# Performance work log

Hardware: AMD Instinct MI355X
Metric: run time of the kernel (lower is better)

The kernel has to match this reference:

```python
import jax, jax.numpy as jnp
import numpy as np

N = 100_000      # nodes
E = 1_600_000    # edges (avg degree 16)
D_IN, D_H, D_OUT = 128, 128, 64


def setup_inputs() -> dict:
    key = jax.random.key(0)
    ks = jax.random.split(key, 6)
    x = jax.random.normal(ks[0], (N, D_IN), jnp.float32)
    edge_index = jax.random.randint(ks[1], (2, E), 0, N, dtype=jnp.int32)
    W1 = jax.random.normal(ks[2], (D_IN, D_H), jnp.float32) / np.sqrt(D_IN)
    b1 = jnp.zeros((D_H,), jnp.float32)
    W2 = jax.random.normal(ks[3], (D_H, D_OUT), jnp.float32) / np.sqrt(D_H)
    b2 = jnp.zeros((D_OUT,), jnp.float32)
    return {"x": x, "edge_index": edge_index, "W1": W1, "b1": b1, "W2": W2, "b2": b2}


def _gcn_layer(x, W, b, src, dst, n_nodes):
    # PyG GCNConv: h = x @ W; symmetric norm with self-loops; scatter-add; + bias
    h = x @ W                                        # [N, D_out]
    deg = jax.ops.segment_sum(jnp.ones_like(dst, jnp.float32), dst,
                              num_segments=n_nodes)  # self-loops => deg >= 1
    dinv = jax.lax.rsqrt(deg)                        # deg^{-1/2}
    norm = dinv[src] * dinv[dst]                     # [E+N]
    msg = h[src] * norm[:, None]                     # gather + scale
    out = jax.ops.segment_sum(msg, dst, num_segments=n_nodes)  # scatter-add
    return out + b


def reference(x, edge_index, W1, b1, W2, b2):
    n = x.shape[0]
    loop = jnp.arange(n, dtype=edge_index.dtype)
    src = jnp.concatenate([edge_index[0], loop])     # add self-loops
    dst = jnp.concatenate([edge_index[1], loop])
    h = _gcn_layer(x, W1, b1, src, dst, n)
    h = jax.nn.relu(h)
    # dropout(p=0.5) is identity in eval mode
    out = _gcn_layer(h, W2, b2, src, dst, n)
    return out
```

## Files before the change

### kernel.cpp

```cpp
#include <hip/hip_runtime.h>
#include <hip/hip_bf16.h>


#define NTHREADS 256
#define BSH 9
#define NBMAX 256

typedef unsigned int uint;
typedef unsigned short ushort;
typedef __attribute__((ext_vector_type(8))) short short8;
typedef __attribute__((ext_vector_type(4))) float floatx4;

__device__ __forceinline__ uint pack_bf16(float a, float b) {
    __hip_bfloat162 h = __float22bfloat162_rn(make_float2(a, b));
    return *reinterpret_cast<uint*>(&h);
}
__device__ __forceinline__ float bf16_lo(uint q) { return __uint_as_float(q << 16); }
__device__ __forceinline__ float bf16_hi(uint q) { return __uint_as_float(q & 0xffff0000u); }

__global__ __launch_bounds__(256) void bucket_hist_kernel(
    const int* __restrict__ dst, int* __restrict__ bcnt, int e, int nb) {
    __shared__ int hist[NBMAX];
    int t = threadIdx.x;
    for (int b = t; b < nb; b += 256) hist[b] = 0;
    __syncthreads();
    int e0 = blockIdx.x * 2048;
#pragma unroll
    for (int v = 0; v < 2; v++) {
        int gi = e0 + t * 8 + v * 4;
        if (gi + 3 < e) {
            int4 d4 = *(const int4*)&dst[gi];
            atomicAdd(&hist[d4.x >> BSH], 1);
            atomicAdd(&hist[d4.y >> BSH], 1);
            atomicAdd(&hist[d4.z >> BSH], 1);
            atomicAdd(&hist[d4.w >> BSH], 1);
        } else {
            for (int j = 0; j < 4; j++)
                if (gi + j < e) atomicAdd(&hist[dst[gi + j] >> BSH], 1);
        }
    }
    __syncthreads();
    for (int b = t; b < nb; b += 256) {
        int v = hist[b];
        if (v) atomicAdd(&bcnt[b], v);
    }
}

__global__ void bucket_scan(const int* __restrict__ bcnt, int* __restrict__ bstart,
                            int* __restrict__ bcursor, int nb) {
    __shared__ int buf[NBMAX];
    int t = threadIdx.x;
    int v = (t < nb) ? bcnt[t] : 0;
    buf[t] = v;
    __syncthreads();
    int x = v;
    for (int off = 1; off < NBMAX; off <<= 1) {
        int y = (t >= off) ? buf[t - off] : 0;
        __syncthreads();
        x += y;
        buf[t] = x;
        __syncthreads();
    }
    if (t < nb) {
        bstart[t] = x - v;
        bcursor[t] = x - v;
    }
}

__global__ __launch_bounds__(256) void partition_kernel(
    const int* __restrict__ src, const int* __restrict__ dst,
    int* __restrict__ bcursor, int2* __restrict__ staged, int e, int nb) {
    __shared__ int eS[2048];
    __shared__ int eD[2048];
    __shared__ int hist[NBMAX];
    __shared__ int base[NBMAX];
    int t = threadIdx.x;
    int e0 = blockIdx.x * 2048;

    for (int b = t; b < nb; b += 256) hist[b] = 0;
    __syncthreads();
#pragma unroll
    for (int v = 0; v < 2; v++) {
        int li = t * 8 + v * 4;
        int gi = e0 + li;
        int4 s4, d4;
        if (gi + 3 < e) {
            s4 = *(const int4*)&src[gi];
            d4 = *(const int4*)&dst[gi];
        } else {
            const int* sp = &src[gi];
            const int* dp = &dst[gi];
            s4.x = (gi + 0 < e) ? sp[0] : 0;  d4.x = (gi + 0 < e) ? dp[0] : -1;
            s4.y = (gi + 1 < e) ? sp[1] : 0;  d4.y = (gi + 1 < e) ? dp[1] : -1;
            s4.z = (gi + 2 < e) ? sp[2] : 0;  d4.z = (gi + 2 < e) ? dp[2] : -1;
            s4.w = (gi + 3 < e) ? sp[3] : 0;  d4.w = (gi + 3 < e) ? dp[3] : -1;
        }
        *(int4*)&eS[li] = s4;
        *(int4*)&eD[li] = d4;
        if (d4.x >= 0) atomicAdd(&hist[d4.x >> BSH], 1);
        if (d4.y >= 0) atomicAdd(&hist[d4.y >> BSH], 1);
        if (d4.z >= 0) atomicAdd(&hist[d4.z >> BSH], 1);
        if (d4.w >= 0) atomicAdd(&hist[d4.w >> BSH], 1);
    }
    __syncthreads();
    for (int b = t; b < nb; b += 256) {
        int v = hist[b];
        base[b] = v ? atomicAdd(&bcursor[b], v) : 0;
        hist[b] = 0;
    }
    __syncthreads();
#pragma unroll
    for (int i = 0; i < 8; i++) {
        int li = t + i * 256;
        int d = eD[li];
        if (d >= 0) {
            int b = d >> BSH;
            int r = atomicAdd(&hist[b], 1);
            staged[base[b] + r] = make_int2(eS[li], d);
        }
    }
}

__global__ __launch_bounds__(256) void fine_count_kernel(
    const int2* __restrict__ staged, const int* __restrict__ bstart,
    const int* __restrict__ bcnt, int* __restrict__ cnt,
    int* __restrict__ startA, float* __restrict__ dinv, int n) {
    __shared__ int lcnt[512];
    __shared__ int tsum[256];
    int b = blockIdx.x;
    int t = threadIdx.x;
    lcnt[t] = 0;
    lcnt[t + 256] = 0;
    __syncthreads();
    int s0 = bstart[b];
    int m = bcnt[b];
    for (int i = t; i < m; i += 256)
        atomicAdd(&lcnt[staged[s0 + i].y & 511], 1);
    __syncthreads();
    int v0 = lcnt[2 * t];
    int v1 = lcnt[2 * t + 1];
    int tot = v0 + v1;
    tsum[t] = tot;
    __syncthreads();
    int x = tot;
    for (int off = 1; off < 256; off <<= 1) {
        int y = (t >= off) ? tsum[t - off] : 0;
        __syncthreads();
        x += y;
        tsum[t] = x;
        __syncthreads();
    }
    int excl = x - tot;
    int node = (b << BSH) + 2 * t;
    if (node < n) {
        cnt[node] = v0;
        startA[node] = s0 + excl;
        dinv[node] = rsqrtf((float)v0 + 1.0f);
    }
    if (node + 1 < n) {
        cnt[node + 1] = v1;
        startA[node + 1] = s0 + excl + v0;
        dinv[node + 1] = rsqrtf((float)v1 + 1.0f);
    }
}

__global__ __launch_bounds__(256) void fine_fill_kernel(
    const int2* __restrict__ staged, const int* __restrict__ bstart,
    const int* __restrict__ bcnt, const int* __restrict__ startA,
    const float* __restrict__ dinv, int2* __restrict__ rec, int n) {
    __shared__ int lcur[512];
    __shared__ float ldv[512];
    int b = blockIdx.x;
    int t = threadIdx.x;
    int nb0 = b << BSH;
    for (int i = t; i < 512; i += 256) {
        int node = nb0 + i;
        lcur[i] = (node < n) ? startA[node] : 0;
        ldv[i] = (node < n) ? dinv[node] : 0.f;
    }
    __syncthreads();
    int s0 = bstart[b];
    int m = bcnt[b];
    for (int i = t; i < m; i += 256) {
        int2 ed = staged[s0 + i];
        int li = ed.y & 511;
        int pos = atomicAdd(&lcur[li], 1);
        float nw = dinv[ed.x] * ldv[li];
        rec[pos] = make_int2(ed.x, __float_as_int(nw));
    }
}

template <int COLS, bool XF32>
__global__ __launch_bounds__(256) void gemm_mfma(const void* __restrict__ Xv,
                                                 const float* __restrict__ W,
                                                 uint* __restrict__ Cq, int n) {
    __shared__ ushort sX[64 * 128];
    __shared__ ushort sWT[COLS * 128];
    int t = threadIdx.x;
    int rbase = blockIdx.x * 64;

    if (XF32) {
        const float* X = (const float*)Xv;
#pragma unroll
        for (int i = 0; i < 8; i++) {
            int f = t + 256 * i;
            int r = f >> 5;
            int c4 = f & 31;
            float4 v = make_float4(0.f, 0.f, 0.f, 0.f);
            int gr = rbase + r;
            if (gr < n) v = *(const float4*)(X + (size_t)gr * 128 + c4 * 4);
            uint lo = pack_bf16(v.x, v.y);
            uint hi = pack_bf16(v.z, v.w);
            int chunk = c4 >> 1;
            int sub = (c4 & 1) * 4;
            int off = r * 128 + (((chunk ^ (r & 15)) << 3) + sub);
            *(uint2*)&sX[off] = make_uint2(lo, hi);
        }
    } else {
        const ushort* X = (const ushort*)Xv;
#pragma unroll
        for (int i = 0; i < 4; i++) {
            int f = t + 256 * i;
            int r = f >> 4;
            int chunk = f & 15;
            uint4 v = make_uint4(0, 0, 0, 0);
            int gr = rbase + r;
            if (gr < n) v = *(const uint4*)(X + (size_t)gr * 128 + chunk * 8);
            int off = r * 128 + ((chunk ^ (r & 15)) << 3);
            *(uint4*)&sX[off] = v;
        }
    }
    {
        constexpr int UNITS = 64 * (COLS / 4);
        constexpr int PER_T = UNITS / 256;
#pragma unroll
        for (int i = 0; i < PER_T; i++) {
            int u = t + 256 * i;
            int kp = u / (COLS / 4);
            int n4 = u % (COLS / 4);
            int k = kp * 2;
            float4 w0 = *(const float4*)(W + (size_t)k * COLS + n4 * 4);
            float4 w1 = *(const float4*)(W + (size_t)(k + 1) * COLS + n4 * 4);
            int chunk = k >> 3;
            int sub = k & 7;
            const float* a0 = (const float*)&w0;
            const float* a1 = (const float*)&w1;
#pragma unroll
            for (int j = 0; j < 4; j++) {
                int nn = n4 * 4 + j;
                uint pk = pack_bf16(a0[j], a1[j]);
                int off = nn * 128 + (((chunk ^ (nn & 15)) << 3) + sub);
                *(uint*)&sWT[off] = pk;
            }
        }
    }
    __syncthreads();

    int lane = t & 63;
    int wave = t >> 6;
    int m = lane & 15;
    int q = lane >> 4;
    int r0 = wave * 16;

    floatx4 acc[COLS / 16];
#pragma unroll
    for (int c = 0; c < COLS / 16; c++) acc[c] = (floatx4){0.f, 0.f, 0.f, 0.f};

#pragma unroll
    for (int ks = 0; ks < 4; ks++) {
        int rr = r0 + m;
        int ca = (ks * 4 + q) ^ (rr & 15);
        short8 afrag = *(const short8*)&sX[rr * 128 + (ca << 3)];
#pragma unroll
        for (int c = 0; c < COLS / 16; c++) {
            int nn = c * 16 + m;
            int cb = (ks * 4 + q) ^ (nn & 15);
            short8 bfrag = *(const short8*)&sWT[nn * 128 + (cb << 3)];
            acc[c] = __builtin_amdgcn_mfma_f32_16x16x32_bf16(bfrag, afrag, acc[c], 0, 0, 0);
        }
    }

    int gr = rbase + r0 + m;
    if (gr < n) {
#pragma unroll
        for (int c = 0; c < COLS / 16; c++) {
            uint2 pk;
            pk.x = pack_bf16(acc[c][0], acc[c][1]);
            pk.y = pack_bf16(acc[c][2], acc[c][3]);
            *(uint2*)&Cq[(size_t)gr * (COLS / 2) + c * 8 + q * 2] = pk;
        }
    }
}

__global__ __launch_bounds__(256) void aggregate128q(
    const uint* __restrict__ hq, const int2* __restrict__ rec,
    const int* __restrict__ start, const int* __restrict__ cnt,
    const float* __restrict__ dinv, const float* __restrict__ bias,
    uint* __restrict__ outq, int n) {
    int w = (int)((blockIdx.x * blockDim.x + threadIdx.x) >> 6);
    if (w >= n) return;
    int lane = threadIdx.x & 63;
    int half = lane >> 5;
    int fl = lane & 31;
    const uint2* h2 = (const uint2*)hq;

    float a0 = 0.f, a1 = 0.f, a2 = 0.f, a3 = 0.f;
    float di = dinv[w];
    if (half == 0) {
        uint2 q = h2[(size_t)w * 32 + fl];
        float sw = di * di;
        a0 = bf16_lo(q.x) * sw; a1 = bf16_hi(q.x) * sw;
        a2 = bf16_lo(q.y) * sw; a3 = bf16_hi(q.y) * sw;
    }
    int j0 = __builtin_amdgcn_readfirstlane(start[w]);
    int deg = __builtin_amdgcn_readfirstlane(cnt[w]);
    const int2* rp = rec + j0;

    int t = 0;
    for (; t + 16 <= deg; t += 16) {
        uint2 q[8]; float wf[8];
#pragma unroll
        for (int u = 0; u < 8; u++) {
            int2 ea = rp[t + 2 * u];
            int2 eb = rp[t + 2 * u + 1];
            int s = half ? eb.x : ea.x;
            wf[u] = __int_as_float(half ? eb.y : ea.y);
            q[u] = h2[(size_t)s * 32 + fl];
        }
#pragma unroll
        for (int u = 0; u < 8; u++) {
            a0 += bf16_lo(q[u].x) * wf[u]; a1 += bf16_hi(q[u].x) * wf[u];
            a2 += bf16_lo(q[u].y) * wf[u]; a3 += bf16_hi(q[u].y) * wf[u];
        }
    }
    for (; t + 4 <= deg; t += 4) {
        uint2 q[2]; float wf[2];
#pragma unroll
        for (int u = 0; u < 2; u++) {
            int2 ea = rp[t + 2 * u];
            int2 eb = rp[t + 2 * u + 1];
            int s = half ? eb.x : ea.x;
            wf[u] = __int_as_float(half ? eb.y : ea.y);
            q[u] = h2[(size_t)s * 32 + fl];
        }
#pragma unroll
        for (int u = 0; u < 2; u++) {
            a0 += bf16_lo(q[u].x) * wf[u]; a1 += bf16_hi(q[u].x) * wf[u];
            a2 += bf16_lo(q[u].y) * wf[u]; a3 += bf16_hi(q[u].y) * wf[u];
        }
    }
    for (; t < deg; t += 2) {
        int2 ea = rp[t];
        int2 eb = (t + 1 < deg) ? rp[t + 1] : make_int2(0, 0);
        int s = half ? eb.x : ea.x;
        float wfv = __int_as_float(half ? eb.y : ea.y);
        uint2 q = h2[(size_t)s * 32 + fl];
        a0 += bf16_lo(q.x) * wfv; a1 += bf16_hi(q.x) * wfv;
        a2 += bf16_lo(q.y) * wfv; a3 += bf16_hi(q.y) * wfv;
    }

    a0 += __shfl(a0, lane ^ 32);
    a1 += __shfl(a1, lane ^ 32);
    a2 += __shfl(a2, lane ^ 32);
    a3 += __shfl(a3, lane ^ 32);
    if (half == 0) {
        float4 bb = *(const float4*)&bias[4 * fl];
        float o0 = fmaxf(a0 + bb.x, 0.f);
        float o1 = fmaxf(a1 + bb.y, 0.f);
        float o2 = fmaxf(a2 + bb.z, 0.f);
        float o3 = fmaxf(a3 + bb.w, 0.f);
        uint2 pk;
        pk.x = pack_bf16(o0, o1);
        pk.y = pack_bf16(o2, o3);
        *(uint2*)&outq[(size_t)w * 64 + fl * 2] = pk;
    }
}

__global__ __launch_bounds__(256) void aggregate64q(
    const ushort* __restrict__ hq, const int2* __restrict__ rec,
    const int* __restrict__ start, const int* __restrict__ cnt,
    const float* __restrict__ dinv, const float* __restrict__ bias,
    float* __restrict__ out, int n) {
    int w = (int)((blockIdx.x * blockDim.x + threadIdx.x) >> 6);
    if (w >= n) return;
    int lane = threadIdx.x & 63;
    int half = lane >> 5;
    int fl = lane & 31;
    const uint* h2 = (const uint*)hq;

    float a0 = 0.f, a1 = 0.f;
    float di = dinv[w];
    if (half == 0) {
        uint q = h2[(size_t)w * 32 + fl];
        float sw = di * di;
        a0 = bf16_lo(q) * sw;
        a1 = bf16_hi(q) * sw;
    }
    int j0 = __builtin_amdgcn_readfirstlane(start[w]);
    int deg = __builtin_amdgcn_readfirstlane(cnt[w]);
    const int2* rp = rec + j0;

    int t = 0;
    for (; t + 16 <= deg; t += 16) {
        uint q[8]; float wf[8];
#pragma unroll
        for (int u = 0; u < 8; u++) {
            int2 ea = rp[t + 2 * u];
            int2 eb = rp[t + 2 * u + 1];
            int s = half ? eb.x : ea.x;
            wf[u] = __int_as_float(half ? eb.y : ea.y);
            q[u] = h2[(size_t)s * 32 + fl];
        }
#pragma unroll
        for (int u = 0; u < 8; u++) {
            a0 += bf16_lo(q[u]) * wf[u];
            a1 += bf16_hi(q[u]) * wf[u];
        }
    }
    for (; t + 4 <= deg; t += 4) {
        uint q[2]; float wf[2];
#pragma unroll
        for (int u = 0; u < 2; u++) {
            int2 ea = rp[t + 2 * u];
            int2 eb = rp[t + 2 * u + 1];
            int s = half ? eb.x : ea.x;
            wf[u] = __int_as_float(half ? eb.y : ea.y);
            q[u] = h2[(size_t)s * 32 + fl];
        }
#pragma unroll
        for (int u = 0; u < 2; u++) {
            a0 += bf16_lo(q[u]) * wf[u];
            a1 += bf16_hi(q[u]) * wf[u];
        }
    }
    for (; t < deg; t += 2) {
        int2 ea = rp[t];
        int2 eb = (t + 1 < deg) ? rp[t + 1] : make_int2(0, 0);
        int s = half ? eb.x : ea.x;
        float wfv = __int_as_float(half ? eb.y : ea.y);
        uint q = h2[(size_t)s * 32 + fl];
        a0 += bf16_lo(q) * wfv;
        a1 += bf16_hi(q) * wfv;
    }

    a0 += __shfl(a0, lane ^ 32);
    a1 += __shfl(a1, lane ^ 32);
    if (half == 0) {
        float2 bb = *(const float2*)&bias[2 * fl];
        float2 o;
        o.x = a0 + bb.x;
        o.y = a1 + bb.y;
        ((float2*)out)[(size_t)w * 32 + fl] = o;
    }
}

extern "C" void kernel_launch(void* const* d_in, const int* in_sizes, int n_in,
                              void* d_out, int out_size, void* d_ws, size_t ws_size,
                              hipStream_t stream) {
    const float* x = (const float*)d_in[0];
    const int* edge = (const int*)d_in[1];
    const float* W1 = (const float*)d_in[2];
    const float* b1 = (const float*)d_in[3];
    const float* W2 = (const float*)d_in[4];
    const float* b2 = (const float*)d_in[5];

    const int N = in_sizes[0] / 128;
    const int E = in_sizes[1] / 2;
    const int* src = edge;
    const int* dst = edge + E;
    const int NB = (N + (1 << BSH) - 1) >> BSH;

    char* p = (char*)d_ws;
    int* cnt = (int*)p;       p += (size_t)N * 4;
    int* startA = (int*)p;    p += (size_t)N * 4;
    int* bcnt = (int*)p;      p += NBMAX * 4;
    int* bstart = (int*)p;    p += NBMAX * 4;
    int* bcursor = (int*)p;   p += NBMAX * 4;
    float* dinv = (float*)p;  p += (size_t)N * 4;
    int2* rec = (int2*)p;     p += (size_t)E * 8;
    uint* hq = (uint*)p;      p += (size_t)N * 64 * 4;
    uint* g = (uint*)p;       p += (size_t)N * 64 * 4;
    ushort* h2q = (ushort*)p; p += (size_t)N * 64 * 2;

    int2* staged = (int2*)g;

    float* out = (float*)d_out;
    const int eblocks = (E + 2047) / 2048;

    (void)hipMemsetAsync(bcnt, 0, NBMAX * 4, stream);
    bucket_hist_kernel<<<eblocks, 256, 0, stream>>>(dst, bcnt, E, NB);
    bucket_scan<<<1, NBMAX, 0, stream>>>(bcnt, bstart, bcursor, NB);
    partition_kernel<<<eblocks, 256, 0, stream>>>(src, dst, bcursor, staged, E, NB);
    fine_count_kernel<<<NB, 256, 0, stream>>>(staged, bstart, bcnt, cnt, startA, dinv, N);
    fine_fill_kernel<<<NB, 256, 0, stream>>>(staged, bstart, bcnt, startA, dinv, rec, N);

    const int gblocks = (N + 63) / 64;

    gemm_mfma<128, true><<<gblocks, 256, 0, stream>>>(x, W1, hq, N);
    aggregate128q<<<(N + 3) / 4, 256, 0, stream>>>(hq, rec, startA, cnt, dinv, b1, g, N);

    gemm_mfma<64, false><<<gblocks, 256, 0, stream>>>(g, W2, (uint*)h2q, N);
    aggregate64q<<<(N + 3) / 4, 256, 0, stream>>>(h2q, rec, startA, cnt, dinv, b2, out, N);
}
```

Measured before the change: 323.6 us.

## Assign one node per half-wave in aggregation and pack per-node metadata

The aggregation kernels now give each 32-lane half of a wave its own destination node, instead of splitting one node's edges across the two halves and combining them with shuffles. The per-node start offset, degree and squared self-loop weight are packed into one int4 metadata record written by the count kernel, so a single load replaces three separate loads. This removes the cross-half reduction and should balance degree variance better, but each node's neighbor gathers now run in a single half-wave. Because the two halves of a wave can have different degrees, the wave may diverge, and edge loads are no longer uniform across the wave.

New measurement: 320.2 us. About the same (-1.0%).

```diff
diff --git a/kernel.cpp b/kernel.cpp
--- a/kernel.cpp
+++ b/kernel.cpp
@@ -123,7 +123,7 @@
 
 __global__ __launch_bounds__(256) void fine_count_kernel(
     const int2* __restrict__ staged, const int* __restrict__ bstart,
-    const int* __restrict__ bcnt, int* __restrict__ cnt,
+    const int* __restrict__ bcnt, int4* __restrict__ meta,
     int* __restrict__ startA, float* __restrict__ dinv, int n) {
     __shared__ int lcnt[512];
     __shared__ int tsum[256];
@@ -153,14 +153,16 @@
     int excl = x - tot;
     int node = (b << BSH) + 2 * t;
     if (node < n) {
-        cnt[node] = v0;
+        float di = rsqrtf((float)v0 + 1.0f);
         startA[node] = s0 + excl;
-        dinv[node] = rsqrtf((float)v0 + 1.0f);
+        dinv[node] = di;
+        meta[node] = make_int4(s0 + excl, v0, __float_as_int(di * di), 0);
     }
     if (node + 1 < n) {
-        cnt[node + 1] = v1;
+        float di = rsqrtf((float)v1 + 1.0f);
         startA[node + 1] = s0 + excl + v0;
-        dinv[node + 1] = rsqrtf((float)v1 + 1.0f);
+        dinv[node + 1] = di;
+        meta[node + 1] = make_int4(s0 + excl + v0, v1, __float_as_int(di * di), 0);
     }
 }
 
@@ -294,38 +296,31 @@
 
 __global__ __launch_bounds__(256) void aggregate128q(
     const uint* __restrict__ hq, const int2* __restrict__ rec,
-    const int* __restrict__ start, const int* __restrict__ cnt,
-    const float* __restrict__ dinv, const float* __restrict__ bias,
+    const int4* __restrict__ meta, const float* __restrict__ bias,
     uint* __restrict__ outq, int n) {
-    int w = (int)((blockIdx.x * blockDim.x + threadIdx.x) >> 6);
+    int w = (int)((blockIdx.x * blockDim.x + threadIdx.x) >> 5);
     if (w >= n) return;
-    int lane = threadIdx.x & 63;
-    int half = lane >> 5;
-    int fl = lane & 31;
+    int fl = threadIdx.x & 31;
     const uint2* h2 = (const uint2*)hq;
 
-    float a0 = 0.f, a1 = 0.f, a2 = 0.f, a3 = 0.f;
-    float di = dinv[w];
-    if (half == 0) {
-        uint2 q = h2[(size_t)w * 32 + fl];
-        float sw = di * di;
-        a0 = bf16_lo(q.x) * sw; a1 = bf16_hi(q.x) * sw;
-        a2 = bf16_lo(q.y) * sw; a3 = bf16_hi(q.y) * sw;
-    }
-    int j0 = __builtin_amdgcn_readfirstlane(start[w]);
-    int deg = __builtin_amdgcn_readfirstlane(cnt[w]);
+    int4 mt = meta[w];
+    int j0 = mt.x;
+    int deg = mt.y;
+    float swq = __int_as_float(mt.z);
+
+    uint2 qs = h2[(size_t)w * 32 + fl];
+    float a0 = bf16_lo(qs.x) * swq, a1 = bf16_hi(qs.x) * swq;
+    float a2 = bf16_lo(qs.y) * swq, a3 = bf16_hi(qs.y) * swq;
+
     const int2* rp = rec + j0;
-
     int t = 0;
-    for (; t + 16 <= deg; t += 16) {
+    for (; t + 8 <= deg; t += 8) {
         uint2 q[8]; float wf[8];
 #pragma unroll
         for (int u = 0; u < 8; u++) {
-            int2 ea = rp[t + 2 * u];
-            int2 eb = rp[t + 2 * u + 1];
-            int s = half ? eb.x : ea.x;
-            wf[u] = __int_as_float(half ? eb.y : ea.y);
-            q[u] = h2[(size_t)s * 32 + fl];
+            int2 e = rp[t + u];
+            wf[u] = __int_as_float(e.y);
+            q[u] = h2[(size_t)e.x * 32 + fl];
         }
 #pragma unroll
         for (int u = 0; u < 8; u++) {
@@ -333,83 +328,62 @@
             a2 += bf16_lo(q[u].y) * wf[u]; a3 += bf16_hi(q[u].y) * wf[u];
         }
     }
-    for (; t + 4 <= deg; t += 4) {
-        uint2 q[2]; float wf[2];
-#pragma unroll
-        for (int u = 0; u < 2; u++) {
-            int2 ea = rp[t + 2 * u];
-            int2 eb = rp[t + 2 * u + 1];
-            int s = half ? eb.x : ea.x;
-            wf[u] = __int_as_float(half ? eb.y : ea.y);
-            q[u] = h2[(size_t)s * 32 + fl];
-        }
-#pragma unroll
-        for (int u = 0; u < 2; u++) {
-            a0 += bf16_lo(q[u].x) * wf[u]; a1 += bf16_hi(q[u].x) * wf[u];
-            a2 += bf16_lo(q[u].y) * wf[u]; a3 += bf16_hi(q[u].y) * wf[u];
-        }
-    }
-    for (; t < deg; t += 2) {
-        int2 ea = rp[t];
-        int2 eb = (t + 1 < deg) ? rp[t + 1] : make_int2(0, 0);
-        int s = half ? eb.x : ea.x;
-        float wfv = __int_as_float(half ? eb.y : ea.y);
-        uint2 q = h2[(size_t)s * 32 + fl];
-        a0 += bf16_lo(q.x) * wfv; a1 += bf16_hi(q.x) * wfv;
-        a2 += bf16_lo(q.y) * wfv; a3 += bf16_hi(q.y) * wfv;
-    }
-
-    a0 += __shfl(a0, lane ^ 32);
-    a1 += __shfl(a1, lane ^ 32);
-    a2 += __shfl(a2, lane ^ 32);
-    a3 += __shfl(a3, lane ^ 32);
-    if (half == 0) {
-        float4 bb = *(const float4*)&bias[4 * fl];
-        float o0 = fmaxf(a0 + bb.x, 0.f);
-        float o1 = fmaxf(a1 + bb.y, 0.f);
-        float o2 = fmaxf(a2 + bb.z, 0.f);
-        float o3 = fmaxf(a3 + bb.w, 0.f);
-        uint2 pk;
-        pk.x = pack_bf16(o0, o1);
-        pk.y = pack_bf16(o2, o3);
-        *(uint2*)&outq[(size_t)w * 64 + fl * 2] = pk;
-    }
+    for (; t + 2 <= deg; t += 2) {
+        int2 e0 = rp[t], e1 = rp[t + 1];
+        float w0 = __int_as_float(e0.y), w1 = __int_as_float(e1.y);
+        uint2 q0 = h2[(size_t)e0.x * 32 + fl];
+        uint2 q1 = h2[(size_t)e1.x * 32 + fl];
+        a0 += bf16_lo(q0.x) * w0 + bf16_lo(q1.x) * w1;
+        a1 += bf16_hi(q0.x) * w0 + bf16_hi(q1.x) * w1;
+        a2 += bf16_lo(q0.y) * w0 + bf16_lo(q1.y) * w1;
+        a3 += bf16_hi(q0.y) * w0 + bf16_hi(q1.y) * w1;
+    }
+    if (t < deg) {
+        int2 e = rp[t];
+        float wv = __int_as_float(e.y);
+        uint2 q = h2[(size_t)e.x * 32 + fl];
+        a0 += bf16_lo(q.x) * wv; a1 += bf16_hi(q.x) * wv;
+        a2 += bf16_lo(q.y) * wv; a3 += bf16_hi(q.y) * wv;
+    }
+
+    float4 bb = *(const float4*)&bias[4 * fl];
+    float o0 = fmaxf(a0 + bb.x, 0.f);
+    float o1 = fmaxf(a1 + bb.y, 0.f);
+    float o2 = fmaxf(a2 + bb.z, 0.f);
+    float o3 = fmaxf(a3 + bb.w, 0.f);
+    uint2 pk;
+    pk.x = pack_bf16(o0, o1);
+    pk.y = pack_bf16(o2, o3);
+    *(uint2*)&outq[(size_t)w * 64 + fl * 2] = pk;
 }
 
 __global__ __launch_bounds__(256) void aggregate64q(
     const ushort* __restrict__ hq, const int2* __restrict__ rec,
-    const int* __restrict__ start, const int* __restrict__ cnt,
-    const float* __restrict__ dinv, const float* __restrict__ bias,
+    const int4* __restrict__ meta, const float* __restrict__ bias,
     float* __restrict__ out, int n) {
-    int w = (int)((blockIdx.x * blockDim.x + threadIdx.x) >> 6);
+    int w = (int)((blockIdx.x * blockDim.x + threadIdx.x) >> 5);
     if (w >= n) return;
-    int lane = threadIdx.x & 63;
-    int half = lane >> 5;
-    int fl = lane & 31;
+    int fl = threadIdx.x & 31;
     const uint* h2 = (const uint*)hq;
 
-    float a0 = 0.f, a1 = 0.f;
-    float di = dinv[w];
-    if (half == 0) {
-        uint q = h2[(size_t)w * 32 + fl];
-        float sw = di * di;
-        a0 = bf16_lo(q) * sw;
-        a1 = bf16_hi(q) * sw;
-    }
-    int j0 = __builtin_amdgcn_readfirstlane(start[w]);
-    int deg = __builtin_amdgcn_readfirstlane(cnt[w]);
+    int4 mt = meta[w];
+    int j0 = mt.x;
+    int deg = mt.y;
+    float swq = __int_as_float(mt.z);
+
+    uint qs = h2[(size_t)w * 32 + fl];
+    float a0 = bf16_lo(qs) * swq;
+    float a1 = bf16_hi(qs) * swq;
+
     const int2* rp = rec + j0;
-
     int t = 0;
-    for (; t + 16 <= deg; t += 16) {
+    for (; t + 8 <= deg; t += 8) {
         uint q[8]; float wf[8];
 #pragma unroll
         for (int u = 0; u < 8; u++) {
-            int2 ea = rp[t + 2 * u];
-            int2 eb = rp[t + 2 * u + 1];
-            int s = half ? eb.x : ea.x;
-            wf[u] = __int_as_float(half ? eb.y : ea.y);
-            q[u] = h2[(size_t)s * 32 + fl];
+            int2 e = rp[t + u];
+            wf[u] = __int_as_float(e.y);
+            q[u] = h2[(size_t)e.x * 32 + fl];
         }
 #pragma unroll
         for (int u = 0; u < 8; u++) {
@@ -417,41 +391,27 @@
             a1 += bf16_hi(q[u]) * wf[u];
         }
     }
-    for (; t + 4 <= deg; t += 4) {
-        uint q[2]; float wf[2];
-#pragma unroll
-        for (int u = 0; u < 2; u++) {
-            int2 ea = rp[t + 2 * u];
-            int2 eb = rp[t + 2 * u + 1];
-            int s = half ? eb.x : ea.x;
-            wf[u] = __int_as_float(half ? eb.y : ea.y);
-            q[u] = h2[(size_t)s * 32 + fl];
-        }
-#pragma unroll
-        for (int u = 0; u < 2; u++) {
-            a0 += bf16_lo(q[u]) * wf[u];
-            a1 += bf16_hi(q[u]) * wf[u];
-        }
-    }
-    for (; t < deg; t += 2) {
-        int2 ea = rp[t];
-        int2 eb = (t + 1 < deg) ? rp[t + 1] : make_int2(0, 0);
-        int s = half ? eb.x : ea.x;
-        float wfv = __int_as_float(half ? eb.y : ea.y);
-        uint q = h2[(size_t)s * 32 + fl];
-        a0 += bf16_lo(q) * wfv;
-        a1 += bf16_hi(q) * wfv;
-    }
-
-    a0 += __shfl(a0, lane ^ 32);
-    a1 += __shfl(a1, lane ^ 32);
-    if (half == 0) {
-        float2 bb = *(const float2*)&bias[2 * fl];
-        float2 o;
-        o.x = a0 + bb.x;
-        o.y = a1 + bb.y;
-        ((float2*)out)[(size_t)w * 32 + fl] = o;
-    }
+    for (; t + 2 <= deg; t += 2) {
+        int2 e0 = rp[t], e1 = rp[t + 1];
+        float w0 = __int_as_float(e0.y), w1 = __int_as_float(e1.y);
+        uint q0 = h2[(size_t)e0.x * 32 + fl];
+        uint q1 = h2[(size_t)e1.x * 32 + fl];
+        a0 += bf16_lo(q0) * w0 + bf16_lo(q1) * w1;
+        a1 += bf16_hi(q0) * w0 + bf16_hi(q1) * w1;
+    }
+    if (t < deg) {
+        int2 e = rp[t];
+        float wv = __int_as_float(e.y);
+        uint q = h2[(size_t)e.x * 32 + fl];
+        a0 += bf16_lo(q) * wv;
+        a1 += bf16_hi(q) * wv;
+    }
+
+    float2 bb = *(const float2*)&bias[2 * fl];
+    float2 o;
+    o.x = a0 + bb.x;
+    o.y = a1 + bb.y;
+    ((float2*)out)[(size_t)w * 32 + fl] = o;
 }
 
 extern "C" void kernel_launch(void* const* d_in, const int* in_sizes, int n_in,
@@ -471,12 +431,12 @@
     const int NB = (N + (1 << BSH) - 1) >> BSH;
 
     char* p = (char*)d_ws;
-    int* cnt = (int*)p;       p += (size_t)N * 4;
     int* startA = (int*)p;    p += (size_t)N * 4;
     int* bcnt = (int*)p;      p += NBMAX * 4;
     int* bstart = (int*)p;    p += NBMAX * 4;
     int* bcursor = (int*)p;   p += NBMAX * 4;
     float* dinv = (float*)p;  p += (size_t)N * 4;
+    int4* meta = (int4*)p;    p += (size_t)N * 16;
     int2* rec = (int2*)p;     p += (size_t)E * 8;
     uint* hq = (uint*)p;      p += (size_t)N * 64 * 4;
     uint* g = (uint*)p;       p += (size_t)N * 64 * 4;
@@ -491,14 +451,15 @@
     bucket_hist_kernel<<<eblocks, 256, 0, stream>>>(dst, bcnt, E, NB);
     bucket_scan<<<1, NBMAX, 0, stream>>>(bcnt, bstart, bcursor, NB);
     partition_kernel<<<eblocks, 256, 0, stream>>>(src, dst, bcursor, staged, E, NB);
-    fine_count_kernel<<<NB, 256, 0, stream>>>(staged, bstart, bcnt, cnt, startA, dinv, N);
+    fine_count_kernel<<<NB, 256, 0, stream>>>(staged, bstart, bcnt, meta, startA, dinv, N);
     fine_fill_kernel<<<NB, 256, 0, stream>>>(staged, bstart, bcnt, startA, dinv, rec, N);
 
     const int gblocks = (N + 63) / 64;
+    const int ablocks = (N + 7) / 8;
 
     gemm_mfma<128, true><<<gblocks, 256, 0, stream>>>(x, W1, hq, N);
-    aggregate128q<<<(N + 3) / 4, 256, 0, stream>>>(hq, rec, startA, cnt, dinv, b1, g, N);
+    aggregate128q<<<ablocks, 256, 0, stream>>>(hq, rec, meta, b1, g, N);
 
     gemm_mfma<64, false><<<gblocks, 256, 0, stream>>>(g, W2, (uint*)h2q, N);
-    aggregate64q<<<(N + 3) / 4, 256, 0, stream>>>(h2q, rec, startA, cnt, dinv, b2, out, N);
-}
+    aggregate64q<<<ablocks, 256, 0, stream>>>(h2q, rec, meta, b2, out, N);
+}
```
